# Kernel tuning notes

Measured on AMD Instinct MI355X. Metric: run time of the kernel, lower is better.

## Reference

```python
import jax, jax.numpy as jnp
import numpy as np

T0, TBAR, TPOINTS, STEP = 0.0, 2.0, 10, 0.1
N_GRID = int(np.ceil((TBAR - T0) / STEP)) + 1  # 21 internal RK4 grid points (torchdiffeq fixed-grid)
B, N, D_IN, D_HID, D_FF, D_MLP, D_OUT = 256, 100, 3, 256, 1024, 128, 2


def _linear_params(key, fan_in, fan_out):
    # torch.nn.Linear default init: U(-1/sqrt(fan_in), 1/sqrt(fan_in))
    bound = 1.0 / np.sqrt(fan_in)
    kw, kb = jax.random.split(key)
    W = jax.random.uniform(kw, (fan_out, fan_in), minval=-bound, maxval=bound, dtype=jnp.float32)
    b = jax.random.uniform(kb, (fan_out,), minval=-bound, maxval=bound, dtype=jnp.float32)
    return W, b


def setup_inputs() -> dict:
    key = jax.random.key(0)
    kx, k1, k2, k3, k4 = jax.random.split(key, 5)
    w1_W, w1_b = _linear_params(k1, D_IN, D_HID)
    w2_W, w2_b = _linear_params(k2, D_HID, D_FF)
    w3_W, w3_b = _linear_params(k3, D_FF + D_HID, D_MLP)
    out_W, out_b = _linear_params(k4, D_MLP, D_OUT)
    return dict(
        x=jax.random.normal(kx, (B, N, D_IN), dtype=jnp.float32),
        w1_W=w1_W, w1_b=w1_b,
        w2_W=w2_W, w2_b=w2_b,
        w3_W=w3_W, w3_b=w3_b,
        out_W=out_W, out_b=out_b,
        wpool_w=jnp.ones((TPOINTS,), dtype=jnp.float32),
    )


def reference(x, w1_W, w1_b, w2_W, w2_b, w3_W, w3_b, out_W, out_b, wpool_w):
    feature = jax.nn.relu(x @ w1_W.T + w1_b)              # [B, N, 256]
    gamma = feature

    def f(p):  # nmODE dynamics (time-independent)
        return -p + jnp.sin(p + gamma) ** 2

    h = jnp.float32(STEP)

    def rk4_step(y, _):
        k1 = f(y)
        k2 = f(y + 0.5 * h * k1)
        k3 = f(y + 0.5 * h * k2)
        k4 = f(y + h * k3)
        y1 = y + (h / 6.0) * (k1 + 2.0 * k2 + 2.0 * k3 + k4)
        return y1, y1

    y0 = jnp.zeros_like(feature)
    _, ys_tail = jax.lax.scan(rk4_step, y0, None, length=N_GRID - 1)
    ys = jnp.concatenate([y0[None], ys_tail], axis=0)     # [21, B, N, 256]

    # torchdiffeq interpolates fixed-grid solution linearly at the requested timepoints
    tt = np.linspace(T0, TBAR, TPOINTS)
    pos = tt / STEP
    idx = np.minimum(np.floor(pos).astype(np.int32), N_GRID - 2)
    frac = (pos - idx).astype(np.float32)[:, None, None, None]
    yt = ys[idx] * (1.0 - frac) + ys[idx + 1] * frac      # [10, B, N, 256]

    # WeightedAveragePooling over timepoints
    w = jax.nn.softmax(wpool_w)
    yt = jnp.einsum('t,tbnd->bnd', w, yt)                 # [B, N, 256]

    x2 = jax.nn.relu(feature @ w2_W.T + w2_b)             # [B, N, 1024]
    x2 = jnp.max(x2, axis=1, keepdims=True)               # [B, 1, 1024]
    x2 = jnp.broadcast_to(x2, (x2.shape[0], feature.shape[1], x2.shape[2]))
    h3 = jax.nn.relu(jnp.concatenate([x2, yt], axis=2) @ w3_W.T + w3_b)  # [B, N, 128]
    return h3 @ out_W.T + out_b                           # [B, N, 2]
```

## Files before the change

### kernel.cpp

```cpp
#include <hip/hip_runtime.h>

typedef __bf16 bf16x8 __attribute__((ext_vector_type(8)));
typedef float f32x4 __attribute__((ext_vector_type(4)));
typedef unsigned short u16x8 __attribute__((ext_vector_type(8)));

#define MFMA16(a, b, c) __builtin_amdgcn_mfma_f32_16x16x32_bf16((a), (b), (c), 0, 0, 0)

#define INVPI 0.31830988618379067f
#define TBL_N 4096
#define TBL_SCALE 409.6f
#define TBL_STEP (10.f / 4096.f)

__device__ __forceinline__ unsigned short f2bf(float f) {
    unsigned int u = __float_as_uint(f);
    u = u + 0x7FFFu + ((u >> 16) & 1u);
    return (unsigned short)(u >> 16);
}

__device__ __forceinline__ float feval(float y, float gp) {
    float u = fmaf(y, INVPI, gp);
    float cc = __builtin_amdgcn_cosf(u);
    return fmaf(-0.5f, cc, 0.5f - y);
}

__global__ void k_prep(const float* __restrict__ w2W, const float* __restrict__ w3W,
                       const float* __restrict__ wp,
                       unsigned short* __restrict__ w2bf, unsigned short* __restrict__ w3bbf,
                       float* __restrict__ tbl, float* __restrict__ w3aT) {
    int blk = blockIdx.x;
    if (blk < 128) {
        int i = (blk * 256 + threadIdx.x) * 8;
        const float4* s4 = reinterpret_cast<const float4*>(w2W + i);
        float4 a = s4[0], b = s4[1];
        u16x8 o;
        o[0] = f2bf(a.x); o[1] = f2bf(a.y); o[2] = f2bf(a.z); o[3] = f2bf(a.w);
        o[4] = f2bf(b.x); o[5] = f2bf(b.y); o[6] = f2bf(b.z); o[7] = f2bf(b.w);
        *reinterpret_cast<u16x8*>(w2bf + i) = o;
        return;
    }
    if (blk < 144) {
        int idx = ((blk - 128) * 256 + threadIdx.x) * 8;
        int j = idx >> 8, dk = idx & 255;
        const float4* s4 = reinterpret_cast<const float4*>(w3W + j * 1280 + 1024 + dk);
        float4 a = s4[0], b = s4[1];
        u16x8 o;
        o[0] = f2bf(a.x); o[1] = f2bf(a.y); o[2] = f2bf(a.z); o[3] = f2bf(a.w);
        o[4] = f2bf(b.x); o[5] = f2bf(b.y); o[6] = f2bf(b.z); o[7] = f2bf(b.w);
        *reinterpret_cast<u16x8*>(w3bbf + idx) = o;
        return;
    }
    if (blk < 160) {
        int gid = (blk - 144) * 256 + threadIdx.x;

        float c[21];
#pragma unroll
        for (int g = 0; g < 21; ++g) c[g] = 0.f;
        {
            float wv[10];
#pragma unroll
            for (int t = 0; t < 10; ++t) wv[t] = wp[t];
            float m = wv[0];
#pragma unroll
            for (int t = 1; t < 10; ++t) m = fmaxf(m, wv[t]);
            float s = 0.f;
#pragma unroll
            for (int t = 0; t < 10; ++t) { wv[t] = __expf(wv[t] - m); s += wv[t]; }
            float inv = 1.f / s;
            const int   idxs[10]  = {0, 2, 4, 6, 8, 11, 13, 15, 17, 19};
            const float fracs[10] = {0.f, 0.22222222f, 0.44444445f, 0.6666667f, 0.8888889f,
                                     0.11111111f, 0.33333334f, 0.5555556f, 0.7777778f, 1.0f};
#pragma unroll
            for (int t = 0; t < 10; ++t) {
                float w = wv[t] * inv;
                c[idxs[t]]     += w * (1.f - fracs[t]);
                c[idxs[t] + 1] += w * fracs[t];
            }
        }

        float gamma = gid * TBL_STEP;
        float gp = gamma * INVPI;
        float y = 0.f, acc = 0.f;
#pragma unroll
        for (int st = 0; st < 20; ++st) {
            float k1 = feval(y, gp);
            float k2 = feval(fmaf(0.05f, k1, y), gp);
            float k3 = feval(fmaf(0.05f, k2, y), gp);
            float k4 = feval(fmaf(0.1f,  k3, y), gp);
            float sm = k1 + k4;
            sm = fmaf(2.f, k2, sm);
            sm = fmaf(2.f, k3, sm);
            y  = fmaf(0.1f / 6.0f, sm, y);
            acc = fmaf(c[st + 1], y, acc);
        }
        tbl[gid] = acc;
        return;
    }
    {
        int i = (blk - 160) * 256 + threadIdx.x;
        int c = i & 1023, j = i >> 10;
        w3aT[c * 128 + j] = w3W[j * 1280 + c];
    }
}

__global__ void __launch_bounds__(512) k_batch(
    const float* __restrict__ x, const float* __restrict__ w1W, const float* __restrict__ w1b,
    const float* __restrict__ tbl,
    const unsigned short* __restrict__ w2bf, const float* __restrict__ w2b,
    const float* __restrict__ w3aT, const float* __restrict__ w3b,
    const unsigned short* __restrict__ w3bbf,
    const float* __restrict__ outW, const float* __restrict__ outb,
    float* __restrict__ out) {

    __shared__ __align__(1024) char smemA[57344];
    __shared__ __align__(1024) char smemY[57344];
    __shared__ float tl[TBL_N];
    __shared__ float w1s[1024];
    __shared__ float xs[1024];
    __shared__ float ps[4][128];
    __shared__ float vs[128];
    __shared__ float ps2[4][128][2];

    const int b = blockIdx.x;
    const int t = threadIdx.x;

    {
        const float4* g4 = reinterpret_cast<const float4*>(tbl);
        float4* l4 = reinterpret_cast<float4*>(tl);
        l4[t] = g4[t];
        l4[t + 512] = g4[t + 512];
        if (t < 192)
            reinterpret_cast<float4*>(w1s)[t] = reinterpret_cast<const float4*>(w1W)[t];
        else if (t >= 256 && t < 320)
            reinterpret_cast<float4*>(w1s + 768)[t - 256] =
                reinterpret_cast<const float4*>(w1b)[t - 256];
    }
    __syncthreads();

    {
        const float* xb = x + (size_t)b * 300;
#pragma unroll
        for (int i = 0; i < 7; ++i) {
            int k = t + i * 512;
            int row = k >> 5, ch = k & 31;
            int byte = row * 512 + ((ch * 16) ^ ((row & 7) << 4));
            if (row < 100) {
                float x0 = xb[row * 3], x1 = xb[row * 3 + 1], x2 = xb[row * 3 + 2];
                int d0 = ch * 8;
                u16x8 fv, yv;
#pragma unroll
                for (int j = 0; j < 8; ++j) {
                    int d = d0 + j;
                    float g = fmaf(x0, w1s[d * 3],
                              fmaf(x1, w1s[d * 3 + 1],
                              fmaf(x2, w1s[d * 3 + 2], w1s[768 + d])));
                    g = fmaxf(g, 0.f);
                    fv[j] = f2bf(g);
                    float tt = g * TBL_SCALE;
                    int ii = (int)tt;
                    ii = (ii > TBL_N - 2) ? (TBL_N - 2) : ii;
                    float fr = tt - (float)ii;
                    float a0 = tl[ii], a1 = tl[ii + 1];
                    yv[j] = f2bf(fmaf(fr, a1 - a0, a0));
                }
                *reinterpret_cast<u16x8*>(smemA + byte) = fv;
                *reinterpret_cast<u16x8*>(smemY + byte) = yv;
            } else {
                *reinterpret_cast<f32x4*>(smemA + byte) = (f32x4){0.f, 0.f, 0.f, 0.f};
                *reinterpret_cast<f32x4*>(smemY + byte) = (f32x4){0.f, 0.f, 0.f, 0.f};
            }
        }
    }
    __syncthreads();

    const int wave = t >> 6, lane = t & 63;
    const int col16 = lane & 15, krow = lane >> 4;
    const int sw = (col16 & 7) << 4;

#pragma unroll 1
    for (int q = 0; q < 2; ++q) {
        int colbase = q * 512 + wave * 64;
        const unsigned short* bp = w2bf + (size_t)(colbase + col16) * 256 + krow * 8;

        f32x4 acc[7][4];
#pragma unroll
        for (int mt = 0; mt < 7; ++mt)
#pragma unroll
            for (int ct = 0; ct < 4; ++ct) acc[mt][ct] = (f32x4){0.f, 0.f, 0.f, 0.f};

        bf16x8 Bcur[4], Bnxt[4];
#pragma unroll
        for (int ct = 0; ct < 4; ++ct)
            Bcur[ct] = *reinterpret_cast<const bf16x8*>(bp + ct * 4096);

#pragma unroll
        for (int k0 = 0; k0 < 8; ++k0) {
            int off = (k0 * 64 + krow * 16) ^ sw;
            bf16x8 Af[7];
#pragma unroll
            for (int mt = 0; mt < 7; ++mt)
                Af[mt] = *reinterpret_cast<const bf16x8*>(smemA + (mt * 16 + col16) * 512 + off);
            if (k0 < 7) {
#pragma unroll
                for (int ct = 0; ct < 4; ++ct)
                    Bnxt[ct] = *reinterpret_cast<const bf16x8*>(bp + ct * 4096 + (k0 + 1) * 32);
            }
#pragma unroll
            for (int mt = 0; mt < 7; ++mt)
#pragma unroll
                for (int ct = 0; ct < 4; ++ct)
                    acc[mt][ct] = MFMA16(Af[mt], Bcur[ct], acc[mt][ct]);
#pragma unroll
            for (int ct = 0; ct < 4; ++ct) Bcur[ct] = Bnxt[ct];
        }

        float bias[4], m[4];
#pragma unroll
        for (int ct = 0; ct < 4; ++ct) {
            bias[ct] = w2b[colbase + ct * 16 + col16];
            m[ct] = 0.f;
        }
#pragma unroll
        for (int mt = 0; mt < 7; ++mt) {
#pragma unroll
            for (int r = 0; r < 4; ++r) {
                bool valid = (mt * 16 + krow * 4 + r) < 100;
#pragma unroll
                for (int ct = 0; ct < 4; ++ct) {
                    float v = fmaxf(acc[mt][ct][r] + bias[ct], 0.f);
                    if (valid) m[ct] = fmaxf(m[ct], v);
                }
            }
        }
#pragma unroll
        for (int ct = 0; ct < 4; ++ct) {
            m[ct] = fmaxf(m[ct], __shfl_xor(m[ct], 16));
            m[ct] = fmaxf(m[ct], __shfl_xor(m[ct], 32));
        }
        if (lane < 16) {
#pragma unroll
            for (int ct = 0; ct < 4; ++ct)
                xs[colbase + ct * 16 + lane] = m[ct];
        }
    }
    __syncthreads();

    {
        int j = t & 127, cq = t >> 7;
        const float* wt = w3aT + (size_t)cq * 256 * 128 + j;
        const float* xc = xs + cq * 256;
        float s0 = 0.f, s1 = 0.f;
#pragma unroll 8
        for (int c = 0; c < 256; c += 2) {
            s0 = fmaf(xc[c],     wt[(size_t)c * 128],       s0);
            s1 = fmaf(xc[c + 1], wt[(size_t)(c + 1) * 128], s1);
        }
        ps[cq][j] = s0 + s1;
    }
    __syncthreads();
    if (t < 128)
        vs[t] = ((ps[0][t] + ps[1][t]) + (ps[2][t] + ps[3][t])) + w3b[t];

    f32x4 hacc[7];
#pragma unroll
    for (int mt = 0; mt < 7; ++mt) hacc[mt] = (f32x4){0.f, 0.f, 0.f, 0.f};
    {
        const unsigned short* bp4 = w3bbf + (size_t)(wave * 16 + col16) * 256 + krow * 8;
        bf16x8 B4cur = *reinterpret_cast<const bf16x8*>(bp4);
        bf16x8 B4nxt;
#pragma unroll
        for (int k0 = 0; k0 < 8; ++k0) {
            int off = (k0 * 64 + krow * 16) ^ sw;
            bf16x8 Af[7];
#pragma unroll
            for (int mt = 0; mt < 7; ++mt)
                Af[mt] = *reinterpret_cast<const bf16x8*>(smemY + (mt * 16 + col16) * 512 + off);
            if (k0 < 7) B4nxt = *reinterpret_cast<const bf16x8*>(bp4 + (k0 + 1) * 32);
#pragma unroll
            for (int mt = 0; mt < 7; ++mt)
                hacc[mt] = MFMA16(Af[mt], B4cur, hacc[mt]);
            B4cur = B4nxt;
        }
    }
    __syncthreads();

    {
        float* hs = reinterpret_cast<float*>(smemA);
        int col = wave * 16 + col16;
#pragma unroll
        for (int mt = 0; mt < 7; ++mt) {
#pragma unroll
            for (int r = 0; r < 4; ++r) {
                int row = mt * 16 + krow * 4 + r;
                float h = fmaxf(hacc[mt][r] + vs[col], 0.f);
                hs[row * 128 + ((col + row) & 127)] = h;
            }
        }
    }
    __syncthreads();

    {
        const float* hs = reinterpret_cast<const float*>(smemA);
        int rr = t & 127, half = t >> 7;
        float p0 = 0.f, p1 = 0.f;
        if (rr < 112) {
            int j0 = half * 32;
#pragma unroll
            for (int u = 0; u < 32; ++u) {
                int j = j0 + u;
                float h = hs[rr * 128 + ((j + rr) & 127)];
                p0 = fmaf(h, outW[j], p0);
                p1 = fmaf(h, outW[128 + j], p1);
            }
        }
        ps2[half][rr][0] = p0;
        ps2[half][rr][1] = p1;
    }
    __syncthreads();
    if (t < 200) {
        int row = t >> 1, c = t & 1;
        out[((size_t)b * 100 + row) * 2 + c] =
            ((ps2[0][row][c] + ps2[1][row][c]) + (ps2[2][row][c] + ps2[3][row][c])) + outb[c];
    }
}

extern "C" void kernel_launch(void* const* d_in, const int* in_sizes, int n_in,
                              void* d_out, int out_size, void* d_ws, size_t ws_size,
                              hipStream_t stream) {
    const float* x    = (const float*)d_in[0];
    const float* w1W  = (const float*)d_in[1];
    const float* w1b  = (const float*)d_in[2];
    const float* w2W  = (const float*)d_in[3];
    const float* w2b  = (const float*)d_in[4];
    const float* w3W  = (const float*)d_in[5];
    const float* w3b  = (const float*)d_in[6];
    const float* outW = (const float*)d_in[7];
    const float* outb = (const float*)d_in[8];
    const float* wp   = (const float*)d_in[9];
    float* out = (float*)d_out;

    char* ws = (char*)d_ws;
    unsigned short* w2bf_  = (unsigned short*)(ws);
    unsigned short* w3bbf_ = (unsigned short*)(ws + 524288);
    float* tbl             = (float*)(ws + 589824);
    float* w3aT            = (float*)(ws + 606208);

    k_prep<<<672, 256, 0, stream>>>(w2W, w3W, wp, w2bf_, w3bbf_, tbl, w3aT);
    k_batch<<<256, 512, 0, stream>>>(x, w1W, w1b, tbl, w2bf_, w2b, w3aT, w3b,
                                     w3bbf_, outW, outb, out);
}
```

Baseline: 86.74 us.

## Drop w3 transpose prep, use wave-reduced GEMV, widen LDS swizzle

```diff
diff --git a/kernel.cpp b/kernel.cpp
--- a/kernel.cpp
+++ b/kernel.cpp
@@ -26,7 +26,7 @@
 __global__ void k_prep(const float* __restrict__ w2W, const float* __restrict__ w3W,
                        const float* __restrict__ wp,
                        unsigned short* __restrict__ w2bf, unsigned short* __restrict__ w3bbf,
-                       float* __restrict__ tbl, float* __restrict__ w3aT) {
+                       float* __restrict__ tbl) {
     int blk = blockIdx.x;
     if (blk < 128) {
         int i = (blk * 256 + threadIdx.x) * 8;
@@ -49,7 +49,7 @@
         *reinterpret_cast<u16x8*>(w3bbf + idx) = o;
         return;
     }
-    if (blk < 160) {
+    {
         int gid = (blk - 144) * 256 + threadIdx.x;
 
         float c[21];
@@ -93,20 +93,14 @@
             acc = fmaf(c[st + 1], y, acc);
         }
         tbl[gid] = acc;
-        return;
-    }
-    {
-        int i = (blk - 160) * 256 + threadIdx.x;
-        int c = i & 1023, j = i >> 10;
-        w3aT[c * 128 + j] = w3W[j * 1280 + c];
-    }
-}
-
-__global__ void __launch_bounds__(512) k_batch(
+    }
+}
+
+__global__ void __launch_bounds__(512, 2) k_batch(
     const float* __restrict__ x, const float* __restrict__ w1W, const float* __restrict__ w1b,
     const float* __restrict__ tbl,
     const unsigned short* __restrict__ w2bf, const float* __restrict__ w2b,
-    const float* __restrict__ w3aT, const float* __restrict__ w3b,
+    const float* __restrict__ w3W, const float* __restrict__ w3b,
     const unsigned short* __restrict__ w3bbf,
     const float* __restrict__ outW, const float* __restrict__ outb,
     float* __restrict__ out) {
@@ -116,7 +110,6 @@
     __shared__ float tl[TBL_N];
     __shared__ float w1s[1024];
     __shared__ float xs[1024];
-    __shared__ float ps[4][128];
     __shared__ float vs[128];
     __shared__ float ps2[4][128][2];
 
@@ -142,7 +135,7 @@
         for (int i = 0; i < 7; ++i) {
             int k = t + i * 512;
             int row = k >> 5, ch = k & 31;
-            int byte = row * 512 + ((ch * 16) ^ ((row & 7) << 4));
+            int byte = row * 512 + ((ch ^ (row & 15)) << 4);
             if (row < 100) {
                 float x0 = xb[row * 3], x1 = xb[row * 3 + 1], x2 = xb[row * 3 + 2];
                 int d0 = ch * 8;
@@ -174,7 +167,7 @@
 
     const int wave = t >> 6, lane = t & 63;
     const int col16 = lane & 15, krow = lane >> 4;
-    const int sw = (col16 & 7) << 4;
+    const int sw = col16 << 4;
 
 #pragma unroll 1
     for (int q = 0; q < 2; ++q) {
@@ -245,20 +238,20 @@
     __syncthreads();
 
     {
-        int j = t & 127, cq = t >> 7;
-        const float* wt = w3aT + (size_t)cq * 256 * 128 + j;
-        const float* xc = xs + cq * 256;
-        float s0 = 0.f, s1 = 0.f;
-#pragma unroll 8
-        for (int c = 0; c < 256; c += 2) {
-            s0 = fmaf(xc[c],     wt[(size_t)c * 128],       s0);
-            s1 = fmaf(xc[c + 1], wt[(size_t)(c + 1) * 128], s1);
-        }
-        ps[cq][j] = s0 + s1;
-    }
-    __syncthreads();
-    if (t < 128)
-        vs[t] = ((ps[0][t] + ps[1][t]) + (ps[2][t] + ps[3][t])) + w3b[t];
+        int j = wave * 16;
+        for (int jj = 0; jj < 16; ++jj, ++j) {
+            const float* wr = w3W + (size_t)j * 1280;
+            float s = 0.f;
+#pragma unroll
+            for (int cc = 0; cc < 16; ++cc) {
+                int c = cc * 64 + lane;
+                s = fmaf(xs[c], wr[c], s);
+            }
+            s += __shfl_xor(s, 1);  s += __shfl_xor(s, 2);  s += __shfl_xor(s, 4);
+            s += __shfl_xor(s, 8);  s += __shfl_xor(s, 16); s += __shfl_xor(s, 32);
+            if (lane == 0) vs[j] = s + w3b[j];
+        }
+    }
 
     f32x4 hacc[7];
 #pragma unroll
@@ -342,9 +335,8 @@
     unsigned short* w2bf_  = (unsigned short*)(ws);
     unsigned short* w3bbf_ = (unsigned short*)(ws + 524288);
     float* tbl             = (float*)(ws + 589824);
-    float* w3aT            = (float*)(ws + 606208);
-
-    k_prep<<<672, 256, 0, stream>>>(w2W, w3W, wp, w2bf_, w3bbf_, tbl, w3aT);
-    k_batch<<<256, 512, 0, stream>>>(x, w1W, w1b, tbl, w2bf_, w2b, w3aT, w3b,
+
+    k_prep<<<160, 256, 0, stream>>>(w2W, w3W, wp, w2bf_, w3bbf_, tbl);
+    k_batch<<<256, 512, 0, stream>>>(x, w1W, w1b, tbl, w2bf_, w2b, w3W, w3b,
                                      w3bbf_, outW, outb, out);
 }
```

Result: slower. 92.12 us (+6.2%).
